# Kernel tuning notes

Hardware: AMD Instinct MI355X
Metric: run time of the kernel (lower is better)

## Reference

```python
import jax, jax.numpy as jnp
import numpy as np

N = 100000   # num_entities
R = 474      # num_relations (already doubled for inverses)
D = 256      # in_dim == out_dim
E = 1000000  # num edges (first half 'in' mode, second half 'out' mode)
BN_EPS = 1e-5


def setup_inputs() -> dict:
    key = jax.random.key(0)
    ks = jax.random.split(key, 12)
    s = 1.0 / np.sqrt(D)
    return {
        "x": jax.random.normal(ks[0], (N, D), jnp.float32),
        "r": jax.random.normal(ks[1], (R, D), jnp.float32),
        "w_in": jax.random.normal(ks[2], (D, D), jnp.float32) * s,
        "w_out": jax.random.normal(ks[3], (D, D), jnp.float32) * s,
        "w_loop": jax.random.normal(ks[4], (D, D), jnp.float32) * s,
        "w_rel": jax.random.normal(ks[5], (D, D), jnp.float32) * s,
        "loop_rel": jax.random.normal(ks[6], (1, D), jnp.float32),
        "bias": jnp.zeros((D,), jnp.float32),
        "bn_gamma": jnp.ones((D,), jnp.float32),
        "bn_beta": jnp.zeros((D,), jnp.float32),
        "edge_index": jax.random.randint(ks[7], (2, E), 0, N, jnp.int32),
        "edge_type": jax.random.randint(ks[8], (E,), 0, R, jnp.int32),
    }


def reference(x, r, w_in, w_out, w_loop, w_rel, loop_rel, bias,
              bn_gamma, bn_beta, edge_index, edge_type):
    row, col = edge_index[0], edge_index[1]
    # symmetric edge norm 1/(sqrt(D_i) sqrt(D_j)); degrees over all edges
    deg = jax.ops.segment_sum(jnp.ones((E,), x.dtype), row, num_segments=N)
    deg_inv = jnp.where(deg > 0, deg ** -0.5, 0.0)
    norm = deg_inv[row] * deg_inv[col]  # [E]

    r_full = jnp.concatenate([r, loop_rel], axis=0)  # [R+1, D]

    def mode_agg(rw, cl, et, nrm, W):
        # gather -> composition (sub) -> per-mode matmul -> edge-norm -> scatter-add
        composed = x[cl] - r_full[et]                  # [e, D]
        msg = (composed @ W) * nrm[:, None]            # [e, D]
        return jax.ops.segment_sum(msg, rw, num_segments=N)

    half = edge_type.shape[0] // 2
    agg_in = mode_agg(row[:half], col[:half], edge_type[:half], norm[:half], w_in)
    agg_out = mode_agg(row[half:], col[half:], edge_type[half:], norm[half:], w_out)
    # self-loop: every node, relation = loop_rel (no edge norm)
    agg_loop = (x - loop_rel) @ w_loop                 # [N, D]

    h = agg_in + agg_out + agg_loop + bias
    # BatchNorm1d over node dim (batch statistics)
    mean = jnp.mean(h, axis=0)
    var = jnp.var(h, axis=0)
    h = bn_gamma * (h - mean) * jax.lax.rsqrt(var + BN_EPS) + bn_beta
    h = jnp.tanh(h)

    r_out = r @ w_rel  # rel_transformation == 'linear'
    return h, r_out
```

## Files before the change

### kernel.cpp

```cpp
#include <hip/hip_runtime.h>
#include <hip/hip_bf16.h>
#include <stdint.h>

#define D_DIM 256
#define KBIG 768

typedef __attribute__((ext_vector_type(8))) short bf16x8_t;
typedef __attribute__((ext_vector_type(4))) float f32x4_t;

__device__ __forceinline__ float bf2f(uint16_t u) {
    union { uint32_t i; float f; } v; v.i = ((uint32_t)u) << 16; return v.f;
}
__device__ __forceinline__ float blo(uint32_t w) {
    union { uint32_t i; float f; } v; v.i = w << 16; return v.f;
}
__device__ __forceinline__ float bhi(uint32_t w) {
    union { uint32_t i; float f; } v; v.i = w & 0xFFFF0000u; return v.f;
}
__device__ __forceinline__ uint16_t f2bf(float f) {
    union { float f; uint32_t i; } v; v.f = f;
    uint32_t x = v.i;
    uint32_t r = (x + 0x7FFFu + ((x >> 16) & 1u)) >> 16;
    return (uint16_t)r;
}
__device__ __forceinline__ uint32_t pack2(float a, float b) {
    return (uint32_t)f2bf(a) | ((uint32_t)f2bf(b) << 16);
}
__device__ __forceinline__ float loadv(const void* base, int f, size_t idx) {
    return f ? ((const float*)base)[idx] : bf2f(((const uint16_t*)base)[idx]);
}
__device__ __forceinline__ float fast_tanh(float x) {
    float t = __builtin_amdgcn_exp2f(x * 2.8853900817779268f);
    return 1.f - 2.f * __builtin_amdgcn_rcpf(t + 1.f);
}

__device__ __forceinline__ void gll16(const uint16_t* g, uint16_t* l) {
    __builtin_amdgcn_global_load_lds(
        (const __attribute__((address_space(1))) uint32_t*)(const void*)g,
        (__attribute__((address_space(3))) uint32_t*)(void*)l, 16, 0, 0);
}

__global__ void k_detect(const uint32_t* __restrict__ xw, int* __restrict__ flag) {
    __shared__ int cnt[256];
    int t = threadIdx.x;
    int c = 0;
    for (int j = 0; j < 16; j++) {
        uint32_t w = xw[(size_t)(t * 16 + j) * 797];
        uint32_t e = (w >> 7) & 0xFF;
        if (e >= 100 && e <= 140) c++;
    }
    cnt[t] = c;
    __syncthreads();
    for (int off = 128; off > 0; off >>= 1) {
        if (t < off) cnt[t] += cnt[t + off];
        __syncthreads();
    }
    if (t == 0) flag[0] = (cnt[0] < 2048) ? 1 : 0;
}

__global__ __launch_bounds__(256) void k_cast(const void* __restrict__ src,
                                              uint16_t* __restrict__ dst,
                                              int nvec, const int* __restrict__ flagp,
                                              int skip_bf) {
    int f = *flagp;
    int i = blockIdx.x * 256 + threadIdx.x;
    if (i >= nvec) return;
    size_t base = (size_t)i * 8;
    if (f) {
        const float* s = (const float*)src + base;
        float4 a = *(const float4*)s;
        float4 b = *(const float4*)(s + 4);
        uint4 o;
        o.x = (uint32_t)f2bf(a.x) | ((uint32_t)f2bf(a.y) << 16);
        o.y = (uint32_t)f2bf(a.z) | ((uint32_t)f2bf(a.w) << 16);
        o.z = (uint32_t)f2bf(b.x) | ((uint32_t)f2bf(b.y) << 16);
        o.w = (uint32_t)f2bf(b.z) | ((uint32_t)f2bf(b.w) << 16);
        *(uint4*)(dst + base) = o;
    } else {
        if (skip_bf) return;
        *(uint4*)(dst + base) = *(const uint4*)((const uint16_t*)src + base);
    }
}

__global__ void k_transpose(const void* __restrict__ w0, const void* __restrict__ w1,
                            const void* __restrict__ w2, const void* __restrict__ w3,
                            const int* __restrict__ flagp,
                            uint16_t* __restrict__ bt_big, uint16_t* __restrict__ bt_rel) {
    __shared__ uint16_t tile[32][33];
    int f = *flagp;
    int mat = blockIdx.z;
    const void* src = mat == 0 ? w0 : mat == 1 ? w1 : mat == 2 ? w2 : w3;
    int k0 = blockIdx.y * 32, n0 = blockIdx.x * 32;
    int tx = threadIdx.x, ty = threadIdx.y;
    tile[ty][tx] = f2bf(loadv(src, f, (size_t)(k0 + ty) * D_DIM + n0 + tx));
    __syncthreads();
    int n = n0 + ty, k = k0 + tx;
    if (mat < 3) bt_big[(size_t)n * KBIG + mat * D_DIM + k] = tile[tx][ty];
    else         bt_rel[(size_t)n * D_DIM + k] = tile[tx][ty];
}

__global__ void k_cvec(const void* __restrict__ loop_rel, const void* __restrict__ w_loop,
                       const void* __restrict__ bias, const int* __restrict__ flagp,
                       float* __restrict__ cvec) {
    int f = *flagp;
    int c = blockIdx.x;
    int lane = threadIdx.x;
    float s = 0.f;
#pragma unroll
    for (int kk = 0; kk < 4; kk++) {
        int k = kk * 64 + lane;
        s += loadv(loop_rel, f, k) * loadv(w_loop, f, (size_t)k * D_DIM + c);
    }
#pragma unroll
    for (int off = 32; off; off >>= 1) s += __shfl_down(s, off);
    if (lane == 0) cvec[c] = loadv(bias, f, c) - s;
}

__global__ void k_hist(const int* __restrict__ rows, int E, int half,
                       int* __restrict__ deg, int* __restrict__ deg_in) {
    int i = blockIdx.x * blockDim.x + threadIdx.x;
    if (i < E) {
        int r = rows[i];
        atomicAdd(&deg[r], 1);
        if (i < half) atomicAdd(&deg_in[r], 1);
    }
}

__global__ void k_scan_a(const int* __restrict__ deg, int N, int* __restrict__ row_start,
                         int* __restrict__ blk_sum, float* __restrict__ dinv) {
    __shared__ int s[1024];
    int t = threadIdx.x;
    int i = blockIdx.x * 1024 + t;
    int v = (i < N) ? deg[i] : 0;
    if (i < N) dinv[i] = v > 0 ? rsqrtf((float)v) : 0.f;
    s[t] = v;
    __syncthreads();
    for (int off = 1; off < 1024; off <<= 1) {
        int add = (t >= off) ? s[t - off] : 0;
        __syncthreads();
        s[t] += add;
        __syncthreads();
    }
    if (i < N) row_start[i] = s[t] - v;
    if (t == 1023) blk_sum[blockIdx.x] = s[1023];
}

__global__ void k_scan_b(int* __restrict__ blk_sum, int nb) {
    __shared__ int s[128];
    int t = threadIdx.x;
    int v = (t < nb) ? blk_sum[t] : 0;
    s[t] = v;
    __syncthreads();
    for (int off = 1; off < 128; off <<= 1) {
        int add = (t >= off) ? s[t - off] : 0;
        __syncthreads();
        s[t] += add;
        __syncthreads();
    }
    if (t < nb) blk_sum[t] = s[t] - v;
}

__global__ void k_scan_c(int* __restrict__ row_start, const int* __restrict__ blk_sum,
                         const int* __restrict__ deg_in,
                         int N, int E, int* __restrict__ cur_in, int* __restrict__ cur_out) {
    int i = blockIdx.x * 1024 + threadIdx.x;
    if (i < N) {
        int v = row_start[i] + blk_sum[blockIdx.x];
        row_start[i] = v;
        cur_in[i] = v;
        cur_out[i] = v + deg_in[i];
    }
    if (i == 0) row_start[N] = E;
}

__global__ void k_fill(const int* __restrict__ ei, const int* __restrict__ et, int E, int half,
                       int* __restrict__ cur_in, int* __restrict__ cur_out,
                       uint32_t* __restrict__ csr) {
    int e = blockIdx.x * blockDim.x + threadIdx.x;
    if (e >= E) return;
    int r_ = ei[e];
    int c_ = ei[E + e];
    int t_ = et[e];
    uint32_t rec = (uint32_t)c_ | ((uint32_t)t_ << 17);
    int pos = (e < half) ? atomicAdd(&cur_in[r_], 1) : atomicAdd(&cur_out[r_], 1);
    csr[pos] = rec;
}

__global__ __launch_bounds__(256) void k_agg(
    const uint32_t* __restrict__ csr, const int* __restrict__ row_start,
    const int* __restrict__ deg_in, const float* __restrict__ dinv,
    const void* __restrict__ x_raw, const uint16_t* __restrict__ x_bf,
    const uint16_t* __restrict__ r_bf, const int* __restrict__ flagp,
    uint16_t* __restrict__ s_in, uint16_t* __restrict__ s_out, int N) {
    const uint16_t* xs = (*flagp) ? x_bf : (const uint16_t*)x_raw;
    int node = blockIdx.x * 4 + (threadIdx.x >> 6);
    int lane = threadIdx.x & 63;
    if (node >= N) return;
    int half = lane >> 5;
    int co = (lane & 31) * 8;
    int s = row_start[node], e = row_start[node + 1];
    int mid = s + deg_in[node];
    float di = dinv[node];
    float a[8];

#pragma unroll
    for (int k = 0; k < 8; k++) a[k] = 0.f;
    for (int j = s + half; j < mid; j += 2) {
        uint32_t rec = csr[j];
        int c = rec & 131071;
        int et = rec >> 17;
        float nrm = di * dinv[c];
        uint4 xv = *(const uint4*)(xs + ((size_t)c << 8) + co);
        uint4 rv = *(const uint4*)(r_bf + ((size_t)et << 8) + co);
        a[0] = fmaf(blo(xv.x) - blo(rv.x), nrm, a[0]);
        a[1] = fmaf(bhi(xv.x) - bhi(rv.x), nrm, a[1]);
        a[2] = fmaf(blo(xv.y) - blo(rv.y), nrm, a[2]);
        a[3] = fmaf(bhi(xv.y) - bhi(rv.y), nrm, a[3]);
        a[4] = fmaf(blo(xv.z) - blo(rv.z), nrm, a[4]);
        a[5] = fmaf(bhi(xv.z) - bhi(rv.z), nrm, a[5]);
        a[6] = fmaf(blo(xv.w) - blo(rv.w), nrm, a[6]);
        a[7] = fmaf(bhi(xv.w) - bhi(rv.w), nrm, a[7]);
    }
#pragma unroll
    for (int k = 0; k < 8; k++) a[k] += __shfl_xor(a[k], 32);
    if (half == 0) {
        uint4 o;
        o.x = pack2(a[0], a[1]); o.y = pack2(a[2], a[3]);
        o.z = pack2(a[4], a[5]); o.w = pack2(a[6], a[7]);
        *(uint4*)(s_in + (size_t)node * D_DIM + co) = o;
    }

#pragma unroll
    for (int k = 0; k < 8; k++) a[k] = 0.f;
    for (int j = mid + half; j < e; j += 2) {
        uint32_t rec = csr[j];
        int c = rec & 131071;
        int et = rec >> 17;
        float nrm = di * dinv[c];
        uint4 xv = *(const uint4*)(xs + ((size_t)c << 8) + co);
        uint4 rv = *(const uint4*)(r_bf + ((size_t)et << 8) + co);
        a[0] = fmaf(blo(xv.x) - blo(rv.x), nrm, a[0]);
        a[1] = fmaf(bhi(xv.x) - bhi(rv.x), nrm, a[1]);
        a[2] = fmaf(blo(xv.y) - blo(rv.y), nrm, a[2]);
        a[3] = fmaf(bhi(xv.y) - bhi(rv.y), nrm, a[3]);
        a[4] = fmaf(blo(xv.z) - blo(rv.z), nrm, a[4]);
        a[5] = fmaf(bhi(xv.z) - bhi(rv.z), nrm, a[5]);
        a[6] = fmaf(blo(xv.w) - blo(rv.w), nrm, a[6]);
        a[7] = fmaf(bhi(xv.w) - bhi(rv.w), nrm, a[7]);
    }
#pragma unroll
    for (int k = 0; k < 8; k++) a[k] += __shfl_xor(a[k], 32);
    if (half == 1) {
        uint4 o;
        o.x = pack2(a[0], a[1]); o.y = pack2(a[2], a[3]);
        o.z = pack2(a[4], a[5]); o.w = pack2(a[6], a[7]);
        *(uint4*)(s_out + (size_t)node * D_DIM + co) = o;
    }
}

__global__ __launch_bounds__(512) void k_gemm(
    const uint16_t* a0, const uint16_t* a1,
    const uint16_t* a2, const uint16_t* a2alt, const int* __restrict__ flagp,
    int M, const uint16_t* __restrict__ bt, int bstride, int ktot,
    const float* __restrict__ addvec, uint16_t* out,
    float* __restrict__ bn_sum, float* __restrict__ bn_sq) {
    __shared__ uint16_t As[128 * 32];
    __shared__ uint16_t Bs[256 * 32];
    const uint16_t* a2s = (*flagp) ? a2 : a2alt;
    int t = threadIdx.x;
    int mbase = blockIdx.x * 128;
    int wave = t >> 6, lane = t & 63;
    int wm = (wave >> 2) * 64, wn = (wave & 3) * 64;
    int quad = lane >> 4, l15 = lane & 15;

    int roff = lane >> 2, cidx = lane & 3;
    int arowL = wave * 16 + roff;
    int achk = cidx ^ ((arowL >> 1) & 3);
    int agrow = mbase + arowL; if (agrow > M - 1) agrow = M - 1;
    size_t aoff = (size_t)agrow * D_DIM + achk * 8;
    uint16_t* aldsb = &As[(wave * 16) * 32];

    int browL0 = wave * 32 + roff;
    int browL1 = browL0 + 16;
    int bchk0 = cidx ^ ((browL0 >> 1) & 3);
    int bchk1 = cidx ^ ((browL1 >> 1) & 3);
    size_t boff0 = (size_t)browL0 * bstride + bchk0 * 8;
    size_t boff1 = (size_t)browL1 * bstride + bchk1 * 8;
    uint16_t* bldsb0 = &Bs[(wave * 32) * 32];
    uint16_t* bldsb1 = &Bs[(wave * 32 + 16) * 32];

    int afo[4], bfo[4];
#pragma unroll
    for (int im = 0; im < 4; im++) {
        int row = wm + im * 16 + l15;
        afo[im] = row * 32 + (quad ^ ((row >> 1) & 3)) * 8;
    }
#pragma unroll
    for (int in = 0; in < 4; in++) {
        int row = wn + in * 16 + l15;
        bfo[in] = row * 32 + (quad ^ ((row >> 1) & 3)) * 8;
    }

    f32x4_t acc[4][4];
#pragma unroll
    for (int i = 0; i < 4; i++)
#pragma unroll
        for (int j = 0; j < 4; j++) acc[i][j] = (f32x4_t){0.f, 0.f, 0.f, 0.f};

    for (int kt = 0; kt < ktot; kt += 32) {
        const uint16_t* asec = (kt < 256) ? a0 : (kt < 512 ? a1 : a2s);
        int klocal = kt & 255;
        gll16(asec + aoff + klocal, aldsb);
        gll16(bt + boff0 + kt, bldsb0);
        gll16(bt + boff1 + kt, bldsb1);
        __syncthreads();
        bf16x8_t af[4], bfr[4];
#pragma unroll
        for (int im = 0; im < 4; im++) af[im] = *(const bf16x8_t*)(&As[afo[im]]);
#pragma unroll
        for (int in = 0; in < 4; in++) bfr[in] = *(const bf16x8_t*)(&Bs[bfo[in]]);
#pragma unroll
        for (int im = 0; im < 4; im++)
#pragma unroll
            for (int in = 0; in < 4; in++)
                acc[im][in] = __builtin_amdgcn_mfma_f32_16x16x32_bf16(af[im], bfr[in], acc[im][in], 0, 0, 0);
        __syncthreads();
    }

    float s4[4] = {0.f, 0.f, 0.f, 0.f};
    float q4[4] = {0.f, 0.f, 0.f, 0.f};
#pragma unroll
    for (int im = 0; im < 4; im++) {
#pragma unroll
        for (int in = 0; in < 4; in++) {
            int gn = wn + in * 16 + l15;
            float av_ = addvec ? addvec[gn] : 0.f;
#pragma unroll
            for (int i2 = 0; i2 < 4; i2++) {
                int gm = mbase + wm + im * 16 + quad * 4 + i2;
                if (gm < M) {
                    float val = acc[im][in][i2] + av_;
                    out[(size_t)gm * D_DIM + gn] = f2bf(val);
                    if (bn_sum) { s4[in] += val; q4[in] += val * val; }
                }
            }
        }
    }
    if (bn_sum) {
        float* sred = (float*)As;
        if (t < 256) { sred[t] = 0.f; sred[t + 256] = 0.f; }
        __syncthreads();
#pragma unroll
        for (int in = 0; in < 4; in++) {
            float sv = s4[in], qv = q4[in];
            sv += __shfl_xor(sv, 16); sv += __shfl_xor(sv, 32);
            qv += __shfl_xor(qv, 16); qv += __shfl_xor(qv, 32);
            if (quad == 0) {
                int gn = wn + in * 16 + l15;
                atomicAdd(&sred[gn], sv);
                atomicAdd(&sred[gn + 256], qv);
            }
        }
        __syncthreads();
        if (t < 256) {
            atomicAdd(&bn_sum[t], sred[t]);
            atomicAdd(&bn_sq[t], sred[t + 256]);
        }
    }
}

__global__ void k_bnfin(const float* __restrict__ bn_sum, const float* __restrict__ bn_sq,
                        const void* __restrict__ gamma, const void* __restrict__ beta,
                        const int* __restrict__ flagp,
                        int N, float* __restrict__ scale, float* __restrict__ shift) {
    int f = *flagp;
    int c = threadIdx.x;
    float inv_n = 1.f / (float)N;
    float mean = bn_sum[c] * inv_n;
    float var = bn_sq[c] * inv_n - mean * mean;
    float sc = loadv(gamma, f, c) * rsqrtf(var + 1e-5f);
    scale[c] = sc;
    shift[c] = loadv(beta, f, c) - mean * sc;
}

__global__ __launch_bounds__(256) void k_final(const uint16_t* __restrict__ h_pre,
                                               const float* __restrict__ scale,
                                               const float* __restrict__ shift,
                                               const int* __restrict__ flagp,
                                               void* __restrict__ dout, int total) {
    int f = *flagp;
    int t = blockIdx.x * 256 + threadIdx.x;
    int base = t * 8;
    if (base >= total) return;
    int c0 = base & (D_DIM - 1);
    uint4 v = *(const uint4*)(h_pre + base);
    uint16_t e[8];
    e[0] = (uint16_t)(v.x & 0xFFFF); e[1] = (uint16_t)(v.x >> 16);
    e[2] = (uint16_t)(v.y & 0xFFFF); e[3] = (uint16_t)(v.y >> 16);
    e[4] = (uint16_t)(v.z & 0xFFFF); e[5] = (uint16_t)(v.z >> 16);
    e[6] = (uint16_t)(v.w & 0xFFFF); e[7] = (uint16_t)(v.w >> 16);
    float r[8];
#pragma unroll
    for (int i = 0; i < 8; i++)
        r[i] = fast_tanh(bf2f(e[i]) * scale[c0 + i] + shift[c0 + i]);
    if (f) {
        float* fo = (float*)dout + base;
        float4 o0 = {r[0], r[1], r[2], r[3]};
        float4 o1 = {r[4], r[5], r[6], r[7]};
        *(float4*)fo = o0;
        *(float4*)(fo + 4) = o1;
    } else {
        uint4 o;
        o.x = (uint32_t)f2bf(r[0]) | ((uint32_t)f2bf(r[1]) << 16);
        o.y = (uint32_t)f2bf(r[2]) | ((uint32_t)f2bf(r[3]) << 16);
        o.z = (uint32_t)f2bf(r[4]) | ((uint32_t)f2bf(r[5]) << 16);
        o.w = (uint32_t)f2bf(r[6]) | ((uint32_t)f2bf(r[7]) << 16);
        *(uint4*)((uint16_t*)dout + base) = o;
    }
}

__global__ void k_store_r(const uint16_t* __restrict__ stage,
                          const int* __restrict__ flagp,
                          void* __restrict__ dout, size_t off, int cnt) {
    int f = *flagp;
    int i = (blockIdx.x * 256 + threadIdx.x) * 4;
    if (i >= cnt) return;
    ushort4 v = *(const ushort4*)(stage + i);
    if (f) {
        float4 o = {bf2f(v.x), bf2f(v.y), bf2f(v.z), bf2f(v.w)};
        *(float4*)((float*)dout + off + i) = o;
    } else {
        *(ushort4*)((uint16_t*)dout + off + i) = v;
    }
}

extern "C" void kernel_launch(void* const* d_in, const int* in_sizes, int n_in,
                              void* d_out, int out_size, void* d_ws, size_t ws_size,
                              hipStream_t stream) {
    const void* x        = d_in[0];
    const void* r        = d_in[1];
    const void* w_in     = d_in[2];
    const void* w_out    = d_in[3];
    const void* w_loop   = d_in[4];
    const void* w_rel    = d_in[5];
    const void* loop_rel = d_in[6];
    const void* bias     = d_in[7];
    const void* bn_gamma = d_in[8];
    const void* bn_beta  = d_in[9];
    const int* edge_index = (const int*)d_in[10];
    const int* edge_type  = (const int*)d_in[11];

    const int N = in_sizes[0] / D_DIM;
    const int R = in_sizes[1] / D_DIM;
    const int E = in_sizes[11];
    const int half = E / 2;

    char* p = (char*)d_ws;
    auto alloc = [&](size_t bytes) -> void* {
        void* q = (void*)p;
        p += (bytes + 255) & ~(size_t)255;
        return q;
    };
    uint16_t* s_out   = (uint16_t*)alloc((size_t)N * D_DIM * 2);
    uint32_t* csr     = (uint32_t*)alloc((size_t)E * 4);
    uint16_t* bt_big  = (uint16_t*)alloc((size_t)D_DIM * KBIG * 2);
    uint16_t* bt_rel  = (uint16_t*)alloc((size_t)D_DIM * D_DIM * 2);
    uint16_t* r_bf    = (uint16_t*)alloc((size_t)R * D_DIM * 2 + 65536);
    uint16_t* r_stage = (uint16_t*)alloc((size_t)R * D_DIM * 2);
    int*      deg     = (int*)alloc((size_t)N * 4);
    int*      deg_in  = (int*)alloc((size_t)N * 4);
    int*      rstart  = (int*)alloc((size_t)(N + 1) * 4);
    int*      cursor  = (int*)alloc((size_t)N * 4);
    float*    dinv    = (float*)alloc((size_t)N * 4);
    int*      blksum  = (int*)alloc(128 * 4);
    float*    cvec    = (float*)alloc(D_DIM * 4);
    float*    bn_sum  = (float*)alloc(D_DIM * 4);
    float*    bn_sq   = (float*)alloc(D_DIM * 4);
    float*    bscale  = (float*)alloc(D_DIM * 4);
    float*    bshift  = (float*)alloc(D_DIM * 4);
    int*      dflag   = (int*)alloc(256);

    int* cursor_out = deg;

    uint16_t* s_in = (uint16_t*)d_out;
    uint16_t* x_bf = (uint16_t*)d_out + (size_t)N * D_DIM;
    uint16_t* h_pre = s_out;

    hipMemsetAsync(deg, 0, (size_t)N * 4, stream);
    hipMemsetAsync(deg_in, 0, (size_t)N * 4, stream);
    hipMemsetAsync(bn_sum, 0, D_DIM * 4, stream);
    hipMemsetAsync(bn_sq, 0, D_DIM * 4, stream);

    k_detect<<<1, 256, 0, stream>>>((const uint32_t*)x, dflag);
    int xvec = N * D_DIM / 8;
    k_cast<<<(xvec + 255) / 256, 256, 0, stream>>>(x, x_bf, xvec, dflag, 1);
    int rvec = R * D_DIM / 8;
    k_cast<<<(rvec + 255) / 256, 256, 0, stream>>>(r, r_bf, rvec, dflag, 0);
    k_transpose<<<dim3(8, 8, 4), dim3(32, 32), 0, stream>>>(w_in, w_out, w_loop, w_rel,
                                                            dflag, bt_big, bt_rel);
    k_cvec<<<D_DIM, 64, 0, stream>>>(loop_rel, w_loop, bias, dflag, cvec);

    int eb = (E + 255) / 256;
    k_hist<<<eb, 256, 0, stream>>>(edge_index, E, half, deg, deg_in);
    int nb = (N + 1023) / 1024;
    k_scan_a<<<nb, 1024, 0, stream>>>(deg, N, rstart, blksum, dinv);
    k_scan_b<<<1, 128, 0, stream>>>(blksum, nb);
    k_scan_c<<<nb, 1024, 0, stream>>>(rstart, blksum, deg_in, N, E, cursor, cursor_out);
    k_fill<<<eb, 256, 0, stream>>>(edge_index, edge_type, E, half, cursor, cursor_out, csr);

    k_agg<<<(N + 3) / 4, 256, 0, stream>>>(csr, rstart, deg_in, dinv, x, x_bf, r_bf, dflag,
                                           s_in, s_out, N);

    int gx = (N + 127) / 128;
    k_gemm<<<gx, 512, 0, stream>>>(s_in, s_out, x_bf, (const uint16_t*)x, dflag,
                                   N, bt_big, KBIG, KBIG, cvec, h_pre, bn_sum, bn_sq);
    int gr_ = (R + 127) / 128;
    k_gemm<<<gr_, 512, 0, stream>>>(r_bf, r_bf, r_bf, r_bf, dflag,
                                    R, bt_rel, D_DIM, D_DIM, nullptr, r_stage,
                                    nullptr, nullptr);

    k_bnfin<<<1, D_DIM, 0, stream>>>(bn_sum, bn_sq, bn_gamma, bn_beta, dflag, N, bscale, bshift);
    int total = N * D_DIM;
    k_final<<<(total / 8 + 255) / 256, 256, 0, stream>>>(h_pre, bscale, bshift, dflag, d_out, total);
    int rcnt = R * D_DIM;
    k_store_r<<<(rcnt / 4 + 255) / 256, 256, 0, stream>>>(r_stage, dflag, d_out, (size_t)N * D_DIM, rcnt);
}
```

Before: 569.6 us.

## Pack degree counters, precompute edge norms in CSR, packed FMA aggregation, fuse BN finalize

The in-mode and total degree histograms are merged into one atomic per edge by packing both counts into a single int. The CSR record becomes 8 bytes: a premultiplied byte-offset index plus the precomputed edge norm, which removes the dinv gather from the aggregation loop. The aggregation accumulates x and r separately with packed v_pk_fma_f32 and subtracts once at the end. The BN finalize kernel is folded into the final tanh kernel, so every block recomputes scale and shift into shared memory. In exchange, CSR traffic doubles, the offset packing assumes N*512 fits in 32 bits and R < 512, and the in-degree counter is limited to 16 bits.

```diff
diff --git a/kernel.cpp b/kernel.cpp
--- a/kernel.cpp
+++ b/kernel.cpp
@@ -7,15 +7,10 @@
 
 typedef __attribute__((ext_vector_type(8))) short bf16x8_t;
 typedef __attribute__((ext_vector_type(4))) float f32x4_t;
+typedef __attribute__((ext_vector_type(2))) float f32x2_t;
 
 __device__ __forceinline__ float bf2f(uint16_t u) {
     union { uint32_t i; float f; } v; v.i = ((uint32_t)u) << 16; return v.f;
-}
-__device__ __forceinline__ float blo(uint32_t w) {
-    union { uint32_t i; float f; } v; v.i = w << 16; return v.f;
-}
-__device__ __forceinline__ float bhi(uint32_t w) {
-    union { uint32_t i; float f; } v; v.i = w & 0xFFFF0000u; return v.f;
 }
 __device__ __forceinline__ uint16_t f2bf(float f) {
     union { float f; uint32_t i; } v; v.f = f;
@@ -32,6 +27,15 @@
 __device__ __forceinline__ float fast_tanh(float x) {
     float t = __builtin_amdgcn_exp2f(x * 2.8853900817779268f);
     return 1.f - 2.f * __builtin_amdgcn_rcpf(t + 1.f);
+}
+__device__ __forceinline__ f32x2_t up2(uint32_t w) {
+    union { uint32_t u[2]; f32x2_t f; } c;
+    c.u[0] = w << 16;
+    c.u[1] = w & 0xFFFF0000u;
+    return c.f;
+}
+__device__ __forceinline__ void pkfma(f32x2_t& acc, f32x2_t a, f32x2_t b) {
+    asm("v_pk_fma_f32 %0, %1, %2, %0" : "+v"(acc) : "v"(a), "v"(b));
 }
 
 __device__ __forceinline__ void gll16(const uint16_t* g, uint16_t* l) {
@@ -117,13 +121,9 @@
 }
 
 __global__ void k_hist(const int* __restrict__ rows, int E, int half,
-                       int* __restrict__ deg, int* __restrict__ deg_in) {
+                       int* __restrict__ deg) {
     int i = blockIdx.x * blockDim.x + threadIdx.x;
-    if (i < E) {
-        int r = rows[i];
-        atomicAdd(&deg[r], 1);
-        if (i < half) atomicAdd(&deg_in[r], 1);
-    }
+    if (i < E) atomicAdd(&deg[rows[i]], (i < half) ? 0x10001 : 1);
 }
 
 __global__ void k_scan_a(const int* __restrict__ deg, int N, int* __restrict__ row_start,
@@ -131,7 +131,7 @@
     __shared__ int s[1024];
     int t = threadIdx.x;
     int i = blockIdx.x * 1024 + t;
-    int v = (i < N) ? deg[i] : 0;
+    int v = (i < N) ? (deg[i] & 0xFFFF) : 0;
     if (i < N) dinv[i] = v > 0 ? rsqrtf((float)v) : 0.f;
     s[t] = v;
     __syncthreads();
@@ -161,100 +161,99 @@
 }
 
 __global__ void k_scan_c(int* __restrict__ row_start, const int* __restrict__ blk_sum,
-                         const int* __restrict__ deg_in,
+                         const int* __restrict__ degp,
                          int N, int E, int* __restrict__ cur_in, int* __restrict__ cur_out) {
     int i = blockIdx.x * 1024 + threadIdx.x;
     if (i < N) {
         int v = row_start[i] + blk_sum[blockIdx.x];
         row_start[i] = v;
         cur_in[i] = v;
-        cur_out[i] = v + deg_in[i];
+        cur_out[i] = v + (int)(((unsigned)degp[i]) >> 16);
     }
     if (i == 0) row_start[N] = E;
 }
 
 __global__ void k_fill(const int* __restrict__ ei, const int* __restrict__ et, int E, int half,
                        int* __restrict__ cur_in, int* __restrict__ cur_out,
-                       uint32_t* __restrict__ csr) {
+                       const float* __restrict__ dinv, uint2* __restrict__ csr) {
     int e = blockIdx.x * blockDim.x + threadIdx.x;
     if (e >= E) return;
     int r_ = ei[e];
     int c_ = ei[E + e];
     int t_ = et[e];
-    uint32_t rec = (uint32_t)c_ | ((uint32_t)t_ << 17);
+    float w = dinv[r_] * dinv[c_];
+    uint32_t m = ((uint32_t)c_ << 9) | (uint32_t)t_;
     int pos = (e < half) ? atomicAdd(&cur_in[r_], 1) : atomicAdd(&cur_out[r_], 1);
-    csr[pos] = rec;
+    csr[pos] = make_uint2(m, __float_as_uint(w));
 }
 
 __global__ __launch_bounds__(256) void k_agg(
-    const uint32_t* __restrict__ csr, const int* __restrict__ row_start,
-    const int* __restrict__ deg_in, const float* __restrict__ dinv,
+    const uint2* __restrict__ csr, const int* __restrict__ row_start,
+    const int* __restrict__ degp,
     const void* __restrict__ x_raw, const uint16_t* __restrict__ x_bf,
     const uint16_t* __restrict__ r_bf, const int* __restrict__ flagp,
     uint16_t* __restrict__ s_in, uint16_t* __restrict__ s_out, int N) {
-    const uint16_t* xs = (*flagp) ? x_bf : (const uint16_t*)x_raw;
+    const char* xb = (const char*)((*flagp) ? x_bf : (const uint16_t*)x_raw);
+    const char* rb = (const char*)r_bf;
     int node = blockIdx.x * 4 + (threadIdx.x >> 6);
     int lane = threadIdx.x & 63;
     if (node >= N) return;
     int half = lane >> 5;
-    int co = (lane & 31) * 8;
+    int cob = (lane & 31) * 16;
     int s = row_start[node], e = row_start[node + 1];
-    int mid = s + deg_in[node];
-    float di = dinv[node];
+    int mid = s + (int)(((unsigned)degp[node]) >> 16);
+
+    f32x2_t ax[4], ar[4];
     float a[8];
 
 #pragma unroll
-    for (int k = 0; k < 8; k++) a[k] = 0.f;
+    for (int k = 0; k < 4; k++) { ax[k] = (f32x2_t){0.f, 0.f}; ar[k] = (f32x2_t){0.f, 0.f}; }
     for (int j = s + half; j < mid; j += 2) {
-        uint32_t rec = csr[j];
-        int c = rec & 131071;
-        int et = rec >> 17;
-        float nrm = di * dinv[c];
-        uint4 xv = *(const uint4*)(xs + ((size_t)c << 8) + co);
-        uint4 rv = *(const uint4*)(r_bf + ((size_t)et << 8) + co);
-        a[0] = fmaf(blo(xv.x) - blo(rv.x), nrm, a[0]);
-        a[1] = fmaf(bhi(xv.x) - bhi(rv.x), nrm, a[1]);
-        a[2] = fmaf(blo(xv.y) - blo(rv.y), nrm, a[2]);
-        a[3] = fmaf(bhi(xv.y) - bhi(rv.y), nrm, a[3]);
-        a[4] = fmaf(blo(xv.z) - blo(rv.z), nrm, a[4]);
-        a[5] = fmaf(bhi(xv.z) - bhi(rv.z), nrm, a[5]);
-        a[6] = fmaf(blo(xv.w) - blo(rv.w), nrm, a[6]);
-        a[7] = fmaf(bhi(xv.w) - bhi(rv.w), nrm, a[7]);
-    }
+        uint2 rec = csr[j];
+        uint32_t m = rec.x;
+        float w = __uint_as_float(rec.y);
+        uint4 xv = *(const uint4*)(xb + (m & 0xFFFFFE00u) + cob);
+        uint4 rv = *(const uint4*)(rb + ((m & 511u) << 9) + cob);
+        f32x2_t w2 = {w, w};
+        pkfma(ax[0], up2(xv.x), w2); pkfma(ar[0], up2(rv.x), w2);
+        pkfma(ax[1], up2(xv.y), w2); pkfma(ar[1], up2(rv.y), w2);
+        pkfma(ax[2], up2(xv.z), w2); pkfma(ar[2], up2(rv.z), w2);
+        pkfma(ax[3], up2(xv.w), w2); pkfma(ar[3], up2(rv.w), w2);
+    }
+#pragma unroll
+    for (int k = 0; k < 4; k++) { a[2 * k] = ax[k][0] - ar[k][0]; a[2 * k + 1] = ax[k][1] - ar[k][1]; }
 #pragma unroll
     for (int k = 0; k < 8; k++) a[k] += __shfl_xor(a[k], 32);
     if (half == 0) {
         uint4 o;
         o.x = pack2(a[0], a[1]); o.y = pack2(a[2], a[3]);
         o.z = pack2(a[4], a[5]); o.w = pack2(a[6], a[7]);
-        *(uint4*)(s_in + (size_t)node * D_DIM + co) = o;
-    }
-
-#pragma unroll
-    for (int k = 0; k < 8; k++) a[k] = 0.f;
+        *(uint4*)(s_in + (size_t)node * D_DIM + (cob >> 1)) = o;
+    }
+
+#pragma unroll
+    for (int k = 0; k < 4; k++) { ax[k] = (f32x2_t){0.f, 0.f}; ar[k] = (f32x2_t){0.f, 0.f}; }
     for (int j = mid + half; j < e; j += 2) {
-        uint32_t rec = csr[j];
-        int c = rec & 131071;
-        int et = rec >> 17;
-        float nrm = di * dinv[c];
-        uint4 xv = *(const uint4*)(xs + ((size_t)c << 8) + co);
-        uint4 rv = *(const uint4*)(r_bf + ((size_t)et << 8) + co);
-        a[0] = fmaf(blo(xv.x) - blo(rv.x), nrm, a[0]);
-        a[1] = fmaf(bhi(xv.x) - bhi(rv.x), nrm, a[1]);
-        a[2] = fmaf(blo(xv.y) - blo(rv.y), nrm, a[2]);
-        a[3] = fmaf(bhi(xv.y) - bhi(rv.y), nrm, a[3]);
-        a[4] = fmaf(blo(xv.z) - blo(rv.z), nrm, a[4]);
-        a[5] = fmaf(bhi(xv.z) - bhi(rv.z), nrm, a[5]);
-        a[6] = fmaf(blo(xv.w) - blo(rv.w), nrm, a[6]);
-        a[7] = fmaf(bhi(xv.w) - bhi(rv.w), nrm, a[7]);
-    }
+        uint2 rec = csr[j];
+        uint32_t m = rec.x;
+        float w = __uint_as_float(rec.y);
+        uint4 xv = *(const uint4*)(xb + (m & 0xFFFFFE00u) + cob);
+        uint4 rv = *(const uint4*)(rb + ((m & 511u) << 9) + cob);
+        f32x2_t w2 = {w, w};
+        pkfma(ax[0], up2(xv.x), w2); pkfma(ar[0], up2(rv.x), w2);
+        pkfma(ax[1], up2(xv.y), w2); pkfma(ar[1], up2(rv.y), w2);
+        pkfma(ax[2], up2(xv.z), w2); pkfma(ar[2], up2(rv.z), w2);
+        pkfma(ax[3], up2(xv.w), w2); pkfma(ar[3], up2(rv.w), w2);
+    }
+#pragma unroll
+    for (int k = 0; k < 4; k++) { a[2 * k] = ax[k][0] - ar[k][0]; a[2 * k + 1] = ax[k][1] - ar[k][1]; }
 #pragma unroll
     for (int k = 0; k < 8; k++) a[k] += __shfl_xor(a[k], 32);
     if (half == 1) {
         uint4 o;
         o.x = pack2(a[0], a[1]); o.y = pack2(a[2], a[3]);
         o.z = pack2(a[4], a[5]); o.w = pack2(a[6], a[7]);
-        *(uint4*)(s_out + (size_t)node * D_DIM + co) = o;
+        *(uint4*)(s_out + (size_t)node * D_DIM + (cob >> 1)) = o;
     }
 }
 
@@ -369,26 +368,25 @@
     }
 }
 
-__global__ void k_bnfin(const float* __restrict__ bn_sum, const float* __restrict__ bn_sq,
-                        const void* __restrict__ gamma, const void* __restrict__ beta,
-                        const int* __restrict__ flagp,
-                        int N, float* __restrict__ scale, float* __restrict__ shift) {
+__global__ __launch_bounds__(256) void k_final(const uint16_t* __restrict__ h_pre,
+                                               const float* __restrict__ bn_sum,
+                                               const float* __restrict__ bn_sq,
+                                               const void* __restrict__ gamma,
+                                               const void* __restrict__ beta,
+                                               const int* __restrict__ flagp,
+                                               int N, void* __restrict__ dout, int total) {
+    __shared__ float ssc[256], ssh[256];
     int f = *flagp;
-    int c = threadIdx.x;
-    float inv_n = 1.f / (float)N;
-    float mean = bn_sum[c] * inv_n;
-    float var = bn_sq[c] * inv_n - mean * mean;
-    float sc = loadv(gamma, f, c) * rsqrtf(var + 1e-5f);
-    scale[c] = sc;
-    shift[c] = loadv(beta, f, c) - mean * sc;
-}
-
-__global__ __launch_bounds__(256) void k_final(const uint16_t* __restrict__ h_pre,
-                                               const float* __restrict__ scale,
-                                               const float* __restrict__ shift,
-                                               const int* __restrict__ flagp,
-                                               void* __restrict__ dout, int total) {
-    int f = *flagp;
+    {
+        int c = threadIdx.x;
+        float inv_n = 1.f / (float)N;
+        float mean = bn_sum[c] * inv_n;
+        float var = bn_sq[c] * inv_n - mean * mean;
+        float sc = loadv(gamma, f, c) * rsqrtf(var + 1e-5f);
+        ssc[c] = sc;
+        ssh[c] = loadv(beta, f, c) - mean * sc;
+    }
+    __syncthreads();
     int t = blockIdx.x * 256 + threadIdx.x;
     int base = t * 8;
     if (base >= total) return;
@@ -402,7 +400,7 @@
     float r[8];
 #pragma unroll
     for (int i = 0; i < 8; i++)
-        r[i] = fast_tanh(bf2f(e[i]) * scale[c0 + i] + shift[c0 + i]);
+        r[i] = fast_tanh(bf2f(e[i]) * ssc[c0 + i] + ssh[c0 + i]);
     if (f) {
         float* fo = (float*)dout + base;
         float4 o0 = {r[0], r[1], r[2], r[3]};
@@ -462,32 +460,27 @@
         return q;
     };
     uint16_t* s_out   = (uint16_t*)alloc((size_t)N * D_DIM * 2);
-    uint32_t* csr     = (uint32_t*)alloc((size_t)E * 4);
+    uint2*    csr     = (uint2*)alloc((size_t)E * 8);
     uint16_t* bt_big  = (uint16_t*)alloc((size_t)D_DIM * KBIG * 2);
     uint16_t* bt_rel  = (uint16_t*)alloc((size_t)D_DIM * D_DIM * 2);
     uint16_t* r_bf    = (uint16_t*)alloc((size_t)R * D_DIM * 2 + 65536);
     uint16_t* r_stage = (uint16_t*)alloc((size_t)R * D_DIM * 2);
     int*      deg     = (int*)alloc((size_t)N * 4);
-    int*      deg_in  = (int*)alloc((size_t)N * 4);
     int*      rstart  = (int*)alloc((size_t)(N + 1) * 4);
     int*      cursor  = (int*)alloc((size_t)N * 4);
+    int*      cursor_out = (int*)alloc((size_t)N * 4);
     float*    dinv    = (float*)alloc((size_t)N * 4);
     int*      blksum  = (int*)alloc(128 * 4);
     float*    cvec    = (float*)alloc(D_DIM * 4);
     float*    bn_sum  = (float*)alloc(D_DIM * 4);
     float*    bn_sq   = (float*)alloc(D_DIM * 4);
-    float*    bscale  = (float*)alloc(D_DIM * 4);
-    float*    bshift  = (float*)alloc(D_DIM * 4);
     int*      dflag   = (int*)alloc(256);
-
-    int* cursor_out = deg;
 
     uint16_t* s_in = (uint16_t*)d_out;
     uint16_t* x_bf = (uint16_t*)d_out + (size_t)N * D_DIM;
     uint16_t* h_pre = s_out;
 
     hipMemsetAsync(deg, 0, (size_t)N * 4, stream);
-    hipMemsetAsync(deg_in, 0, (size_t)N * 4, stream);
     hipMemsetAsync(bn_sum, 0, D_DIM * 4, stream);
     hipMemsetAsync(bn_sq, 0, D_DIM * 4, stream);
 
@@ -501,14 +494,15 @@
     k_cvec<<<D_DIM, 64, 0, stream>>>(loop_rel, w_loop, bias, dflag, cvec);
 
     int eb = (E + 255) / 256;
-    k_hist<<<eb, 256, 0, stream>>>(edge_index, E, half, deg, deg_in);
+    k_hist<<<eb, 256, 0, stream>>>(edge_index, E, half, deg);
     int nb = (N + 1023) / 1024;
     k_scan_a<<<nb, 1024, 0, stream>>>(deg, N, rstart, blksum, dinv);
     k_scan_b<<<1, 128, 0, stream>>>(blksum, nb);
-    k_scan_c<<<nb, 1024, 0, stream>>>(rstart, blksum, deg_in, N, E, cursor, cursor_out);
-    k_fill<<<eb, 256, 0, stream>>>(edge_index, edge_type, E, half, cursor, cursor_out, csr);
-
-    k_agg<<<(N + 3) / 4, 256, 0, stream>>>(csr, rstart, deg_in, dinv, x, x_bf, r_bf, dflag,
+    k_scan_c<<<nb, 1024, 0, stream>>>(rstart, blksum, deg, N, E, cursor, cursor_out);
+    k_fill<<<eb, 256, 0, stream>>>(edge_index, edge_type, E, half, cursor, cursor_out,
+                                   dinv, csr);
+
+    k_agg<<<(N + 3) / 4, 256, 0, stream>>>(csr, rstart, deg, x, x_bf, r_bf, dflag,
                                            s_in, s_out, N);
 
     int gx = (N + 127) / 128;
@@ -519,9 +513,10 @@
                                     R, bt_rel, D_DIM, D_DIM, nullptr, r_stage,
                                     nullptr, nullptr);
 
-    k_bnfin<<<1, D_DIM, 0, stream>>>(bn_sum, bn_sq, bn_gamma, bn_beta, dflag, N, bscale, bshift);
     int total = N * D_DIM;
-    k_final<<<(total / 8 + 255) / 256, 256, 0, stream>>>(h_pre, bscale, bshift, dflag, d_out, total);
+    k_final<<<(total / 8 + 255) / 256, 256, 0, stream>>>(h_pre, bn_sum, bn_sq,
+                                                         bn_gamma, bn_beta, dflag,
+                                                         N, d_out, total);
     int rcnt = R * D_DIM;
     k_store_r<<<(rcnt / 4 + 255) / 256, 256, 0, stream>>>(r_stage, dflag, d_out, (size_t)N * D_DIM, rcnt);
 }
```

Result: faster. 537.3 us (-5.7%).
